# Kernel optimization log

Measured on AMD Instinct MI355X. Metric: run time of the kernel, lower is better.

Reference implementation:

```python
import jax, jax.numpy as jnp
import numpy as np

N_NODES = 32768
N_EDGES = 524288
N_FEAT = 256
HID = 256
N_GRAPHS = 64
N_CLASSES = 4
NODES_PER_GRAPH = N_NODES // N_GRAPHS
BN_EPS = 1e-5


def setup_inputs() -> dict:
    key = jax.random.key(0)
    ks = jax.random.split(key, 16)
    x = jax.random.normal(ks[0], (N_NODES, N_FEAT), dtype=jnp.float32)
    edge_index = jax.random.randint(ks[1], (2, N_EDGES), 0, N_NODES, dtype=jnp.int32)
    batch = (jnp.arange(N_NODES, dtype=jnp.int32) // NODES_PER_GRAPH)
    def xavier(k, shape):
        fan_in, fan_out = shape[0], shape[1]
        a = float(np.sqrt(6.0 / (fan_in + fan_out)))
        return jax.random.uniform(k, shape, jnp.float32, -a, a)
    return {
        "x": x, "edge_index": edge_index, "batch": batch,
        "W1": xavier(ks[2], (N_FEAT, HID)), "b1": jnp.zeros((HID,), jnp.float32),
        "g1": jnp.ones((HID,), jnp.float32), "be1": jnp.zeros((HID,), jnp.float32),
        "W2": xavier(ks[3], (HID, HID)), "b2": jnp.zeros((HID,), jnp.float32),
        "g2": jnp.ones((HID,), jnp.float32), "be2": jnp.zeros((HID,), jnp.float32),
        "W_ih": xavier(ks[4], (HID, 4 * HID)), "W_hh": xavier(ks[5], (HID, 4 * HID)),
        "b_ih": jnp.zeros((4 * HID,), jnp.float32), "b_hh": jnp.zeros((4 * HID,), jnp.float32),
        "W_fc": xavier(ks[6], (HID, N_CLASSES)), "b_fc": jnp.zeros((N_CLASSES,), jnp.float32),
    }


def gcn_conv(x, W, b, src, dst):
    # PyG GCNConv: add self-loops, symmetric normalization, aggregate, then bias
    h = x @ W                                   # [N, H]
    deg = jnp.zeros((x.shape[0],), h.dtype).at[dst].add(1.0) + 1.0  # in-deg + self-loop
    dinv = jax.lax.rsqrt(deg)
    coef = dinv[src] * dinv[dst]                # [E]
    msg = h[src] * coef[:, None]                # gather + scale, [E, H]
    agg = jnp.zeros_like(h).at[dst].add(msg)    # scatter-add
    agg = agg + h * (1.0 / deg)[:, None]        # self-loop term (norm = 1/deg)
    return agg + b


def batch_norm(x, gamma, beta):
    mean = jnp.mean(x, axis=0)
    var = jnp.mean(jnp.square(x - mean), axis=0)  # biased, as torch BN training
    return (x - mean) * jax.lax.rsqrt(var + BN_EPS) * gamma + beta


def reference(x, edge_index, batch, W1, b1, g1, be1, W2, b2, g2, be2,
              W_ih, W_hh, b_ih, b_hh, W_fc, b_fc):
    src, dst = edge_index[0], edge_index[1]
    h = jax.nn.relu(batch_norm(gcn_conv(x, W1, b1, src, dst), g1, be1))
    h = jax.nn.relu(batch_norm(gcn_conv(h, W2, b2, src, dst), g2, be2))
    # global mean pool over graphs
    sums = jax.ops.segment_sum(h, batch, num_segments=N_GRAPHS)
    cnts = jax.ops.segment_sum(jnp.ones((h.shape[0],), h.dtype), batch, num_segments=N_GRAPHS)
    pooled = sums / cnts[:, None]               # [G, H]
    # LSTM, seq_len = 1, zero initial state -> single cell step
    h0 = jnp.zeros((N_GRAPHS, HID), h.dtype)
    c0 = jnp.zeros((N_GRAPHS, HID), h.dtype)
    gates = pooled @ W_ih + h0 @ W_hh + b_ih + b_hh  # [G, 4H]
    i, f, g, o = jnp.split(gates, 4, axis=1)
    c1 = jax.nn.sigmoid(f) * c0 + jax.nn.sigmoid(i) * jnp.tanh(g)
    h1 = jax.nn.sigmoid(o) * jnp.tanh(c1)
    logits = h1 @ W_fc + b_fc
    logp = jax.nn.log_softmax(logits, axis=1)
    return (logp, (h1[None], c1[None]))
```

## Files before the change

### kernel.cpp

```cpp
#include <hip/hip_runtime.h>
#include <math.h>

#define N_NODES 32768
#define N_FEAT 256
#define HID 256
#define N_GRAPHS 64
#define NPG 512
#define N_CLASSES 4
#define BN_EPS 1e-5f

typedef __attribute__((ext_vector_type(8))) short bf16x8;
typedef __attribute__((ext_vector_type(4))) float f32x4;

__device__ __forceinline__ ushort f2b(float f) {
    union { float f; uint u; } v; v.f = f;
    uint u = v.u;
    return (ushort)((u + 0x7FFFu + ((u >> 16) & 1u)) >> 16);
}
__device__ __forceinline__ float bflo(uint u) {
    union { uint u; float f; } v; v.u = u << 16;
    return v.f;
}
__device__ __forceinline__ float bfhi(uint u) {
    union { uint u; float f; } v; v.u = u & 0xFFFF0000u;
    return v.f;
}

__global__ void k_count(const int* __restrict__ dst, int* __restrict__ degcnt, int E) {
    int e = blockIdx.x * 256 + threadIdx.x;
    if (e < E) atomicAdd(&degcnt[dst[e]], 1);
}

__global__ __launch_bounds__(1024) void k_scan_all(const int* __restrict__ degcnt,
                                                   float* __restrict__ dinv,
                                                   int* __restrict__ row_start,
                                                   int* __restrict__ cursor) {
    __shared__ int wsum[16];
    int t = threadIdx.x;
    int base = t * 32;
    int s = 0;
#pragma unroll
    for (int i = 0; i < 32; ++i) s += degcnt[base + i];
    int lane = t & 63, w = t >> 6;
    int v = s;
    for (int off = 1; off < 64; off <<= 1) {
        int u = __shfl_up(v, off);
        if (lane >= off) v += u;
    }
    if (lane == 63) wsum[w] = v;
    __syncthreads();
    if (t < 16) {
        int x = wsum[t];
        for (int off = 1; off < 16; off <<= 1) {
            int u = __shfl_up(x, off, 16);
            if (t >= off) x += u;
        }
        wsum[t] = x;
    }
    __syncthreads();
    int run = ((w > 0) ? wsum[w - 1] : 0) + v - s;
    for (int i = 0; i < 32; ++i) {
        int n = base + i;
        int c = degcnt[n];
        row_start[n] = run;
        cursor[n] = run;
        dinv[n] = rsqrtf((float)(c + 1));
        run += c;
    }
}

__global__ void k_fill(const int* __restrict__ src, const int* __restrict__ dst,
                       int* __restrict__ cursor, uint* __restrict__ csrs, int E) {
    int e = blockIdx.x * 256 + threadIdx.x;
    if (e >= E) return;
    int d = dst[e];
    int pos = atomicAdd(&cursor[d], 1);
    csrs[pos] = (uint)src[e];
}

__global__ void k_prep(const float* __restrict__ x, ushort* __restrict__ xb, int n8blk,
                       const float* __restrict__ W1, const float* __restrict__ W2,
                       ushort* __restrict__ Wt1, ushort* __restrict__ Wt2) {
    int b = blockIdx.x;
    if (b < n8blk) {
        int i = b * 256 + threadIdx.x;
        float4 v0 = *(const float4*)(x + (size_t)i * 8);
        float4 v1 = *(const float4*)(x + (size_t)i * 8 + 4);
        uint4 o;
        o.x = (uint)f2b(v0.x) | ((uint)f2b(v0.y) << 16);
        o.y = (uint)f2b(v0.z) | ((uint)f2b(v0.w) << 16);
        o.z = (uint)f2b(v1.x) | ((uint)f2b(v1.y) << 16);
        o.w = (uint)f2b(v1.z) | ((uint)f2b(v1.w) << 16);
        *(uint4*)(xb + (size_t)i * 8) = o;
    } else {
        int wb = b - n8blk;
        const float* W = (wb < 256) ? W1 : W2;
        ushort* Wt = (wb < 256) ? Wt1 : Wt2;
        int n = wb & 255;
        int k = threadIdx.x;
        Wt[n * 256 + k] = f2b(W[k * 256 + n]);
    }
}

__global__ __launch_bounds__(256) void k_gemm_bf16(const ushort* __restrict__ A,
                                                   const ushort* __restrict__ Bt,
                                                   const float* __restrict__ dinv,
                                                   ushort* __restrict__ hs) {
    int wid = threadIdx.x >> 6;
    int lane = threadIdx.x & 63;
    int m0 = blockIdx.y * 256 + wid * 64;
    int n0 = blockIdx.x * 64;
    int r = lane & 15;
    int ko = (lane >> 4) * 8;

    const ushort* Ab = A + (size_t)(m0 + r) * 256 + ko;
    const ushort* Bb = Bt + (size_t)(n0 + r) * 256 + ko;

    f32x4 acc[4][4] = {};
#pragma unroll
    for (int ks = 0; ks < 8; ++ks) {
        bf16x8 a[4], b[4];
#pragma unroll
        for (int i = 0; i < 4; ++i) {
            a[i] = *(const bf16x8*)(Ab + i * (16 * 256) + ks * 32);
            b[i] = *(const bf16x8*)(Bb + i * (16 * 256) + ks * 32);
        }
#pragma unroll
        for (int i = 0; i < 4; ++i)
#pragma unroll
            for (int j = 0; j < 4; ++j)
                acc[i][j] = __builtin_amdgcn_mfma_f32_16x16x32_bf16(a[i], b[j], acc[i][j], 0, 0, 0);
    }

    int rr = (lane >> 4) * 4;
    int cc = lane & 15;
#pragma unroll
    for (int i = 0; i < 4; ++i) {
        int row = m0 + i * 16 + rr;
#pragma unroll
        for (int r2 = 0; r2 < 4; ++r2) {
            float dv = dinv[row + r2];
#pragma unroll
            for (int j = 0; j < 4; ++j) {
                int col = n0 + j * 16 + cc;
                int slice = col >> 5;
                int within = col & 31;
                hs[(size_t)slice * (N_NODES * 32) + (size_t)(row + r2) * 32 + within] =
                    f2b(acc[i][j][r2] * dv);
            }
        }
    }
}

__global__ __launch_bounds__(256) void k_agg_bn(const ushort* __restrict__ hs,
                                                const uint* __restrict__ csrs,
                                                const int* __restrict__ row_start,
                                                const int* __restrict__ degcnt,
                                                const float* __restrict__ dinv,
                                                const float* __restrict__ bias,
                                                float* __restrict__ agg,
                                                float* __restrict__ bnsum,
                                                float* __restrict__ bnsq) {
    int slice = blockIdx.x & 7;
    int grp = blockIdx.x >> 3;
    int wid = threadIdx.x >> 6;
    int lane = threadIdx.x & 63;
    int j8 = lane >> 3;
    int fp = lane & 7;
    const ushort* hS = hs + (size_t)slice * (N_NODES * 32);

    float b0 = 0.f, b1 = 0.f, b2 = 0.f, b3 = 0.f;
    if (j8 == 0) {
        b0 = bias[slice * 32 + fp * 4 + 0];
        b1 = bias[slice * 32 + fp * 4 + 1];
        b2 = bias[slice * 32 + fp * 4 + 2];
        b3 = bias[slice * 32 + fp * 4 + 3];
    }

    float st[8] = {0.f, 0.f, 0.f, 0.f, 0.f, 0.f, 0.f, 0.f};

    for (int t = 0; t < 8; ++t) {
        int n = grp * 32 + wid * 8 + t;
        float dv = dinv[n];
        int base = row_start[n];
        int cnt = degcnt[n];
        float a0 = 0.f, a1 = 0.f, a2 = 0.f, a3 = 0.f;
        if (j8 == 0) {
            uint2 hv = *(const uint2*)(hS + (size_t)n * 32 + fp * 4);
            a0 = bflo(hv.x); a1 = bfhi(hv.x);
            a2 = bflo(hv.y); a3 = bfhi(hv.y);
        }
        int j = j8;
        for (; j + 8 < cnt; j += 16) {
            uint s0 = csrs[base + j];
            uint s1 = csrs[base + j + 8];
            uint2 h0 = *(const uint2*)(hS + (size_t)s0 * 32 + fp * 4);
            uint2 h1 = *(const uint2*)(hS + (size_t)s1 * 32 + fp * 4);
            a0 += bflo(h0.x) + bflo(h1.x);
            a1 += bfhi(h0.x) + bfhi(h1.x);
            a2 += bflo(h0.y) + bflo(h1.y);
            a3 += bfhi(h0.y) + bfhi(h1.y);
        }
        if (j < cnt) {
            uint s0 = csrs[base + j];
            uint2 h0 = *(const uint2*)(hS + (size_t)s0 * 32 + fp * 4);
            a0 += bflo(h0.x); a1 += bfhi(h0.x);
            a2 += bflo(h0.y); a3 += bfhi(h0.y);
        }
        a0 += __shfl_xor(a0, 8);  a1 += __shfl_xor(a1, 8);
        a2 += __shfl_xor(a2, 8);  a3 += __shfl_xor(a3, 8);
        a0 += __shfl_xor(a0, 16); a1 += __shfl_xor(a1, 16);
        a2 += __shfl_xor(a2, 16); a3 += __shfl_xor(a3, 16);
        a0 += __shfl_xor(a0, 32); a1 += __shfl_xor(a1, 32);
        a2 += __shfl_xor(a2, 32); a3 += __shfl_xor(a3, 32);
        if (j8 == 0) {
            float o0 = a0 * dv + b0;
            float o1 = a1 * dv + b1;
            float o2 = a2 * dv + b2;
            float o3 = a3 * dv + b3;
            *(float4*)&agg[(size_t)n * HID + slice * 32 + fp * 4] = make_float4(o0, o1, o2, o3);
            st[0] += o0; st[1] += o0 * o0;
            st[2] += o1; st[3] += o1 * o1;
            st[4] += o2; st[5] += o2 * o2;
            st[6] += o3; st[7] += o3 * o3;
        }
    }

    __shared__ float ls[4][8][8];
    if (j8 == 0) {
#pragma unroll
        for (int v = 0; v < 8; ++v) ls[wid][fp][v] = st[v];
    }
    __syncthreads();
    if (threadIdx.x < 64) {
        int f = threadIdx.x >> 3, v = threadIdx.x & 7;
        float tsum = ls[0][f][v] + ls[1][f][v] + ls[2][f][v] + ls[3][f][v];
        int feat = slice * 32 + f * 4 + (v >> 1);
        if ((v & 1) == 0) atomicAdd(&bnsum[feat], tsum);
        else              atomicAdd(&bnsq[feat], tsum);
    }
}

__global__ void k_bn_apply_b(const float* __restrict__ x, const float* __restrict__ bnsum,
                             const float* __restrict__ bnsq, const float* __restrict__ gamma,
                             const float* __restrict__ beta, ushort* __restrict__ out) {
    int i = blockIdx.x * 256 + threadIdx.x;
    if (i >= N_NODES * HID / 4) return;
    int f = (i & 63) * 4;
    const float invN = 1.0f / (float)N_NODES;
    float4 v = *(const float4*)(x + (size_t)i * 4);
    float r[4];
    float vv[4] = {v.x, v.y, v.z, v.w};
#pragma unroll
    for (int q = 0; q < 4; ++q) {
        float mean = bnsum[f + q] * invN;
        float var = bnsq[f + q] * invN - mean * mean;
        float t = (vv[q] - mean) * rsqrtf(var + BN_EPS) * gamma[f + q] + beta[f + q];
        r[q] = t > 0.0f ? t : 0.0f;
    }
    uint2 o;
    o.x = (uint)f2b(r[0]) | ((uint)f2b(r[1]) << 16);
    o.y = (uint)f2b(r[2]) | ((uint)f2b(r[3]) << 16);
    *(uint2*)(out + (size_t)i * 4) = o;
}

__global__ __launch_bounds__(256) void k_bn_pool(const float* __restrict__ agg,
                                                 const float* __restrict__ bnsum,
                                                 const float* __restrict__ bnsq,
                                                 const float* __restrict__ gamma,
                                                 const float* __restrict__ beta,
                                                 float* __restrict__ pooled) {
    int g = blockIdx.x >> 4;
    int blk = blockIdx.x & 15;
    int f = threadIdx.x;
    const float invN = 1.0f / (float)N_NODES;
    float mean = bnsum[f] * invN;
    float var = bnsq[f] * invN - mean * mean;
    float sc = rsqrtf(var + BN_EPS) * gamma[f];
    float sh = beta[f] - mean * sc;
    int r0 = g * NPG + blk * 32;
    float s = 0.0f;
#pragma unroll 4
    for (int r = 0; r < 32; ++r) {
        float v = agg[(size_t)(r0 + r) * HID + f] * sc + sh;
        s += v > 0.0f ? v : 0.0f;
    }
    atomicAdd(&pooled[g * HID + f], s);
}

__global__ __launch_bounds__(256) void k_head(const float* __restrict__ pooled,
                                              const float* __restrict__ W_ih,
                                              const float* __restrict__ b_ih,
                                              const float* __restrict__ b_hh,
                                              const float* __restrict__ W_fc,
                                              const float* __restrict__ b_fc,
                                              float* __restrict__ out) {
    __shared__ float p[HID];
    __shared__ float lsum[N_CLASSES][256];
    __shared__ float logits[N_CLASSES];
    int g = blockIdx.x, j = threadIdx.x;
    p[j] = pooled[g * HID + j] * (1.0f / (float)NPG);
    __syncthreads();

    float gi = 0.f, gf = 0.f, gg = 0.f, go = 0.f;
#pragma unroll 4
    for (int k = 0; k < HID; ++k) {
        float pk = p[k];
        const float* w = &W_ih[(size_t)k * (4 * HID) + j];
        gi += pk * w[0];
        gf += pk * w[HID];
        gg += pk * w[2 * HID];
        go += pk * w[3 * HID];
    }
    gi += b_ih[j] + b_hh[j];
    gf += b_ih[HID + j] + b_hh[HID + j];
    gg += b_ih[2 * HID + j] + b_hh[2 * HID + j];
    go += b_ih[3 * HID + j] + b_hh[3 * HID + j];
    (void)gf;

    float si = 1.f / (1.f + expf(-gi));
    float so = 1.f / (1.f + expf(-go));
    float c1 = si * tanhf(gg);
    float h1 = so * tanhf(c1);

    out[N_GRAPHS * N_CLASSES + g * HID + j] = h1;
    out[N_GRAPHS * N_CLASSES + N_GRAPHS * HID + g * HID + j] = c1;

#pragma unroll
    for (int c = 0; c < N_CLASSES; ++c)
        lsum[c][j] = h1 * W_fc[j * N_CLASSES + c];
    __syncthreads();
    for (int s = 128; s > 0; s >>= 1) {
        if (j < s) {
#pragma unroll
            for (int c = 0; c < N_CLASSES; ++c)
                lsum[c][j] += lsum[c][j + s];
        }
        __syncthreads();
    }
    if (j < N_CLASSES) logits[j] = lsum[j][0] + b_fc[j];
    __syncthreads();
    if (j < N_CLASSES) {
        float m = fmaxf(fmaxf(logits[0], logits[1]), fmaxf(logits[2], logits[3]));
        float lse = m + logf(expf(logits[0] - m) + expf(logits[1] - m) +
                             expf(logits[2] - m) + expf(logits[3] - m));
        out[g * N_CLASSES + j] = logits[j] - lse;
    }
}

extern "C" void kernel_launch(void* const* d_in, const int* in_sizes, int n_in,
                              void* d_out, int out_size, void* d_ws, size_t ws_size,
                              hipStream_t stream) {
    const float* x    = (const float*)d_in[0];
    const int*   ei   = (const int*)d_in[1];
    const float* W1   = (const float*)d_in[3];
    const float* b1   = (const float*)d_in[4];
    const float* g1   = (const float*)d_in[5];
    const float* be1  = (const float*)d_in[6];
    const float* W2   = (const float*)d_in[7];
    const float* b2   = (const float*)d_in[8];
    const float* g2   = (const float*)d_in[9];
    const float* be2  = (const float*)d_in[10];
    const float* W_ih = (const float*)d_in[11];
    const float* b_ih = (const float*)d_in[13];
    const float* b_hh = (const float*)d_in[14];
    const float* W_fc = (const float*)d_in[15];
    const float* b_fc = (const float*)d_in[16];
    float* out = (float*)d_out;

    int E = in_sizes[1] / 2;
    const int* src = ei;
    const int* dst = ei + E;

    const size_t MAT = (size_t)N_NODES * HID;
    float*  agg  = (float*)d_ws;
    ushort* xb   = (ushort*)(agg + MAT);
    ushort* hs   = xb + MAT;
    ushort* Wt1  = hs + MAT;
    ushort* Wt2  = Wt1 + 65536;
    float*  dinv = (float*)(Wt2 + 65536);
    int*    row_start = (int*)(dinv + N_NODES);
    int*    cursor    = row_start + N_NODES;
    uint*   csrs      = (uint*)(cursor + N_NODES);
    int*    degcnt = (int*)(csrs + E);
    float*  bn1sum = (float*)(degcnt + N_NODES);
    float*  bn1sq  = bn1sum + HID;
    float*  bn2sum = bn1sq + HID;
    float*  bn2sq  = bn2sum + HID;
    float*  pooled = bn2sq + HID;
    size_t zeroBytes = (size_t)N_NODES * 4 + 4 * HID * 4 + (size_t)N_GRAPHS * HID * 4;

    dim3 blk(256);
    int edgeBlocks = (E + 255) / 256;
    int n8blk = (int)(MAT / 8 / 256);
    int vec4Blocks = (int)(MAT / 4 / 256);
    dim3 gemmGrid(HID / 64, N_NODES / 256);

    hipMemsetAsync(degcnt, 0, zeroBytes, stream);

    k_count<<<edgeBlocks, blk, 0, stream>>>(dst, degcnt, E);
    k_scan_all<<<1, dim3(1024), 0, stream>>>(degcnt, dinv, row_start, cursor);
    k_fill<<<edgeBlocks, blk, 0, stream>>>(src, dst, cursor, csrs, E);
    k_prep<<<n8blk + 512, blk, 0, stream>>>(x, xb, n8blk, W1, W2, Wt1, Wt2);

    k_gemm_bf16<<<gemmGrid, blk, 0, stream>>>(xb, Wt1, dinv, hs);
    k_agg_bn<<<8192, blk, 0, stream>>>(hs, csrs, row_start, degcnt, dinv, b1, agg, bn1sum, bn1sq);
    k_bn_apply_b<<<vec4Blocks, blk, 0, stream>>>(agg, bn1sum, bn1sq, g1, be1, xb);

    k_gemm_bf16<<<gemmGrid, blk, 0, stream>>>(xb, Wt2, dinv, hs);
    k_agg_bn<<<8192, blk, 0, stream>>>(hs, csrs, row_start, degcnt, dinv, b2, agg, bn2sum, bn2sq);
    k_bn_pool<<<N_GRAPHS * 16, blk, 0, stream>>>(agg, bn2sum, bn2sq, g2, be2, pooled);

    k_head<<<N_GRAPHS, blk, 0, stream>>>(pooled, W_ih, b_ih, b_hh, W_fc, b_fc, out);
}
```

Baseline: 309.5 us.

## Use row-major bf16 features with whole-wave rows in aggregation and bf16 agg buffer

Stores the GEMM output row-major (256 features per node) instead of in 32-feature slices, so each wave processes a full node row, with 64 lanes covering 256 features and the edge loop unrolled by 8. This removes the 8x repeated traversal of the CSR indices across slices and the cross-lane shuffle reductions. The pre-BN aggregate is now stored as bf16 instead of fp32, halving its write and read traffic, at some precision cost before batch norm. Row degrees now come from row_start[n+1], so the separate degcnt load is dropped.

New measurement: 449.3 us. 1.45x slower.

```diff
diff --git a/kernel.cpp b/kernel.cpp
--- a/kernel.cpp
+++ b/kernel.cpp
@@ -67,6 +67,7 @@
         dinv[n] = rsqrtf((float)(c + 1));
         run += c;
     }
+    if (t == 0) row_start[N_NODES] = wsum[15];
 }
 
 __global__ void k_fill(const int* __restrict__ src, const int* __restrict__ dst,
@@ -143,10 +144,7 @@
 #pragma unroll
             for (int j = 0; j < 4; ++j) {
                 int col = n0 + j * 16 + cc;
-                int slice = col >> 5;
-                int within = col & 31;
-                hs[(size_t)slice * (N_NODES * 32) + (size_t)(row + r2) * 32 + within] =
-                    f2b(acc[i][j][r2] * dv);
+                hs[(size_t)(row + r2) * 256 + col] = f2b(acc[i][j][r2] * dv);
             }
         }
     }
@@ -155,108 +153,127 @@
 __global__ __launch_bounds__(256) void k_agg_bn(const ushort* __restrict__ hs,
                                                 const uint* __restrict__ csrs,
                                                 const int* __restrict__ row_start,
-                                                const int* __restrict__ degcnt,
                                                 const float* __restrict__ dinv,
                                                 const float* __restrict__ bias,
-                                                float* __restrict__ agg,
+                                                ushort* __restrict__ aggb,
                                                 float* __restrict__ bnsum,
                                                 float* __restrict__ bnsq) {
-    int slice = blockIdx.x & 7;
-    int grp = blockIdx.x >> 3;
     int wid = threadIdx.x >> 6;
     int lane = threadIdx.x & 63;
-    int j8 = lane >> 3;
-    int fp = lane & 7;
-    const ushort* hS = hs + (size_t)slice * (N_NODES * 32);
-
-    float b0 = 0.f, b1 = 0.f, b2 = 0.f, b3 = 0.f;
-    if (j8 == 0) {
-        b0 = bias[slice * 32 + fp * 4 + 0];
-        b1 = bias[slice * 32 + fp * 4 + 1];
-        b2 = bias[slice * 32 + fp * 4 + 2];
-        b3 = bias[slice * 32 + fp * 4 + 3];
-    }
-
-    float st[8] = {0.f, 0.f, 0.f, 0.f, 0.f, 0.f, 0.f, 0.f};
+    int foff = lane * 4;
+
+    float4 bv = *(const float4*)&bias[foff];
+    float bb[4] = {bv.x, bv.y, bv.z, bv.w};
+
+    float s[4] = {0.f, 0.f, 0.f, 0.f};
+    float q[4] = {0.f, 0.f, 0.f, 0.f};
 
     for (int t = 0; t < 8; ++t) {
-        int n = grp * 32 + wid * 8 + t;
+        int n = blockIdx.x * 32 + wid * 8 + t;
         float dv = dinv[n];
         int base = row_start[n];
-        int cnt = degcnt[n];
-        float a0 = 0.f, a1 = 0.f, a2 = 0.f, a3 = 0.f;
-        if (j8 == 0) {
-            uint2 hv = *(const uint2*)(hS + (size_t)n * 32 + fp * 4);
-            a0 = bflo(hv.x); a1 = bfhi(hv.x);
-            a2 = bflo(hv.y); a3 = bfhi(hv.y);
-        }
-        int j = j8;
-        for (; j + 8 < cnt; j += 16) {
+        int cnt = row_start[n + 1] - base;
+
+        uint2 hv = *(const uint2*)(hs + (size_t)n * 256 + foff);
+        float a0 = bflo(hv.x), a1 = bfhi(hv.x), a2 = bflo(hv.y), a3 = bfhi(hv.y);
+
+        int j = 0;
+        for (; j + 8 <= cnt; j += 8) {
+            uint s0 = csrs[base + j + 0];
+            uint s1 = csrs[base + j + 1];
+            uint s2 = csrs[base + j + 2];
+            uint s3 = csrs[base + j + 3];
+            uint s4 = csrs[base + j + 4];
+            uint s5 = csrs[base + j + 5];
+            uint s6 = csrs[base + j + 6];
+            uint s7 = csrs[base + j + 7];
+            uint2 h0 = *(const uint2*)(hs + (size_t)s0 * 256 + foff);
+            uint2 h1 = *(const uint2*)(hs + (size_t)s1 * 256 + foff);
+            uint2 h2 = *(const uint2*)(hs + (size_t)s2 * 256 + foff);
+            uint2 h3 = *(const uint2*)(hs + (size_t)s3 * 256 + foff);
+            uint2 h4 = *(const uint2*)(hs + (size_t)s4 * 256 + foff);
+            uint2 h5 = *(const uint2*)(hs + (size_t)s5 * 256 + foff);
+            uint2 h6 = *(const uint2*)(hs + (size_t)s6 * 256 + foff);
+            uint2 h7 = *(const uint2*)(hs + (size_t)s7 * 256 + foff);
+            a0 += bflo(h0.x) + bflo(h1.x) + bflo(h2.x) + bflo(h3.x)
+                + bflo(h4.x) + bflo(h5.x) + bflo(h6.x) + bflo(h7.x);
+            a1 += bfhi(h0.x) + bfhi(h1.x) + bfhi(h2.x) + bfhi(h3.x)
+                + bfhi(h4.x) + bfhi(h5.x) + bfhi(h6.x) + bfhi(h7.x);
+            a2 += bflo(h0.y) + bflo(h1.y) + bflo(h2.y) + bflo(h3.y)
+                + bflo(h4.y) + bflo(h5.y) + bflo(h6.y) + bflo(h7.y);
+            a3 += bfhi(h0.y) + bfhi(h1.y) + bfhi(h2.y) + bfhi(h3.y)
+                + bfhi(h4.y) + bfhi(h5.y) + bfhi(h6.y) + bfhi(h7.y);
+        }
+        for (; j + 4 <= cnt; j += 4) {
+            uint s0 = csrs[base + j + 0];
+            uint s1 = csrs[base + j + 1];
+            uint s2 = csrs[base + j + 2];
+            uint s3 = csrs[base + j + 3];
+            uint2 h0 = *(const uint2*)(hs + (size_t)s0 * 256 + foff);
+            uint2 h1 = *(const uint2*)(hs + (size_t)s1 * 256 + foff);
+            uint2 h2 = *(const uint2*)(hs + (size_t)s2 * 256 + foff);
+            uint2 h3 = *(const uint2*)(hs + (size_t)s3 * 256 + foff);
+            a0 += bflo(h0.x) + bflo(h1.x) + bflo(h2.x) + bflo(h3.x);
+            a1 += bfhi(h0.x) + bfhi(h1.x) + bfhi(h2.x) + bfhi(h3.x);
+            a2 += bflo(h0.y) + bflo(h1.y) + bflo(h2.y) + bflo(h3.y);
+            a3 += bfhi(h0.y) + bfhi(h1.y) + bfhi(h2.y) + bfhi(h3.y);
+        }
+        for (; j < cnt; ++j) {
             uint s0 = csrs[base + j];
-            uint s1 = csrs[base + j + 8];
-            uint2 h0 = *(const uint2*)(hS + (size_t)s0 * 32 + fp * 4);
-            uint2 h1 = *(const uint2*)(hS + (size_t)s1 * 32 + fp * 4);
-            a0 += bflo(h0.x) + bflo(h1.x);
-            a1 += bfhi(h0.x) + bfhi(h1.x);
-            a2 += bflo(h0.y) + bflo(h1.y);
-            a3 += bfhi(h0.y) + bfhi(h1.y);
-        }
-        if (j < cnt) {
-            uint s0 = csrs[base + j];
-            uint2 h0 = *(const uint2*)(hS + (size_t)s0 * 32 + fp * 4);
+            uint2 h0 = *(const uint2*)(hs + (size_t)s0 * 256 + foff);
             a0 += bflo(h0.x); a1 += bfhi(h0.x);
             a2 += bflo(h0.y); a3 += bfhi(h0.y);
         }
-        a0 += __shfl_xor(a0, 8);  a1 += __shfl_xor(a1, 8);
-        a2 += __shfl_xor(a2, 8);  a3 += __shfl_xor(a3, 8);
-        a0 += __shfl_xor(a0, 16); a1 += __shfl_xor(a1, 16);
-        a2 += __shfl_xor(a2, 16); a3 += __shfl_xor(a3, 16);
-        a0 += __shfl_xor(a0, 32); a1 += __shfl_xor(a1, 32);
-        a2 += __shfl_xor(a2, 32); a3 += __shfl_xor(a3, 32);
-        if (j8 == 0) {
-            float o0 = a0 * dv + b0;
-            float o1 = a1 * dv + b1;
-            float o2 = a2 * dv + b2;
-            float o3 = a3 * dv + b3;
-            *(float4*)&agg[(size_t)n * HID + slice * 32 + fp * 4] = make_float4(o0, o1, o2, o3);
-            st[0] += o0; st[1] += o0 * o0;
-            st[2] += o1; st[3] += o1 * o1;
-            st[4] += o2; st[5] += o2 * o2;
-            st[6] += o3; st[7] += o3 * o3;
-        }
-    }
-
-    __shared__ float ls[4][8][8];
-    if (j8 == 0) {
-#pragma unroll
-        for (int v = 0; v < 8; ++v) ls[wid][fp][v] = st[v];
-    }
+
+        float o0 = a0 * dv + bb[0];
+        float o1 = a1 * dv + bb[1];
+        float o2 = a2 * dv + bb[2];
+        float o3 = a3 * dv + bb[3];
+        ushort4 ov;
+        ov.x = f2b(o0); ov.y = f2b(o1); ov.z = f2b(o2); ov.w = f2b(o3);
+        *(ushort4*)(aggb + (size_t)n * HID + foff) = ov;
+        s[0] += o0; q[0] += o0 * o0;
+        s[1] += o1; q[1] += o1 * o1;
+        s[2] += o2; q[2] += o2 * o2;
+        s[3] += o3; q[3] += o3 * o3;
+    }
+
+    __shared__ float4 ssum[4][64];
+    __shared__ float4 ssq[4][64];
+    ssum[wid][lane] = make_float4(s[0], s[1], s[2], s[3]);
+    ssq[wid][lane] = make_float4(q[0], q[1], q[2], q[3]);
     __syncthreads();
     if (threadIdx.x < 64) {
-        int f = threadIdx.x >> 3, v = threadIdx.x & 7;
-        float tsum = ls[0][f][v] + ls[1][f][v] + ls[2][f][v] + ls[3][f][v];
-        int feat = slice * 32 + f * 4 + (v >> 1);
-        if ((v & 1) == 0) atomicAdd(&bnsum[feat], tsum);
-        else              atomicAdd(&bnsq[feat], tsum);
-    }
-}
-
-__global__ void k_bn_apply_b(const float* __restrict__ x, const float* __restrict__ bnsum,
+        float4 A = ssum[0][lane], B = ssq[0][lane];
+#pragma unroll
+        for (int w = 1; w < 4; ++w) {
+            float4 a2v = ssum[w][lane], b2v = ssq[w][lane];
+            A.x += a2v.x; A.y += a2v.y; A.z += a2v.z; A.w += a2v.w;
+            B.x += b2v.x; B.y += b2v.y; B.z += b2v.z; B.w += b2v.w;
+        }
+        atomicAdd(&bnsum[foff + 0], A.x); atomicAdd(&bnsq[foff + 0], B.x);
+        atomicAdd(&bnsum[foff + 1], A.y); atomicAdd(&bnsq[foff + 1], B.y);
+        atomicAdd(&bnsum[foff + 2], A.z); atomicAdd(&bnsq[foff + 2], B.z);
+        atomicAdd(&bnsum[foff + 3], A.w); atomicAdd(&bnsq[foff + 3], B.w);
+    }
+}
+
+__global__ void k_bn_apply_b(const ushort* __restrict__ x, const float* __restrict__ bnsum,
                              const float* __restrict__ bnsq, const float* __restrict__ gamma,
                              const float* __restrict__ beta, ushort* __restrict__ out) {
     int i = blockIdx.x * 256 + threadIdx.x;
     if (i >= N_NODES * HID / 4) return;
     int f = (i & 63) * 4;
     const float invN = 1.0f / (float)N_NODES;
-    float4 v = *(const float4*)(x + (size_t)i * 4);
+    uint2 v = *(const uint2*)(x + (size_t)i * 4);
+    float vv[4] = {bflo(v.x), bfhi(v.x), bflo(v.y), bfhi(v.y)};
     float r[4];
-    float vv[4] = {v.x, v.y, v.z, v.w};
-#pragma unroll
-    for (int q = 0; q < 4; ++q) {
-        float mean = bnsum[f + q] * invN;
-        float var = bnsq[f + q] * invN - mean * mean;
-        float t = (vv[q] - mean) * rsqrtf(var + BN_EPS) * gamma[f + q] + beta[f + q];
-        r[q] = t > 0.0f ? t : 0.0f;
+#pragma unroll
+    for (int qq = 0; qq < 4; ++qq) {
+        float mean = bnsum[f + qq] * invN;
+        float var = bnsq[f + qq] * invN - mean * mean;
+        float t = (vv[qq] - mean) * rsqrtf(var + BN_EPS) * gamma[f + qq] + beta[f + qq];
+        r[qq] = t > 0.0f ? t : 0.0f;
     }
     uint2 o;
     o.x = (uint)f2b(r[0]) | ((uint)f2b(r[1]) << 16);
@@ -264,7 +281,7 @@
     *(uint2*)(out + (size_t)i * 4) = o;
 }
 
-__global__ __launch_bounds__(256) void k_bn_pool(const float* __restrict__ agg,
+__global__ __launch_bounds__(256) void k_bn_pool(const ushort* __restrict__ aggb,
                                                  const float* __restrict__ bnsum,
                                                  const float* __restrict__ bnsq,
                                                  const float* __restrict__ gamma,
@@ -282,7 +299,7 @@
     float s = 0.0f;
 #pragma unroll 4
     for (int r = 0; r < 32; ++r) {
-        float v = agg[(size_t)(r0 + r) * HID + f] * sc + sh;
+        float v = bflo((uint)aggb[(size_t)(r0 + r) * HID + f]) * sc + sh;
         s += v > 0.0f ? v : 0.0f;
     }
     atomicAdd(&pooled[g * HID + f], s);
@@ -373,14 +390,14 @@
     const int* dst = ei + E;
 
     const size_t MAT = (size_t)N_NODES * HID;
-    float*  agg  = (float*)d_ws;
-    ushort* xb   = (ushort*)(agg + MAT);
+    ushort* aggb = (ushort*)d_ws;
+    ushort* xb   = aggb + MAT;
     ushort* hs   = xb + MAT;
     ushort* Wt1  = hs + MAT;
     ushort* Wt2  = Wt1 + 65536;
     float*  dinv = (float*)(Wt2 + 65536);
     int*    row_start = (int*)(dinv + N_NODES);
-    int*    cursor    = row_start + N_NODES;
+    int*    cursor    = row_start + N_NODES + 1;
     uint*   csrs      = (uint*)(cursor + N_NODES);
     int*    degcnt = (int*)(csrs + E);
     float*  bn1sum = (float*)(degcnt + N_NODES);
@@ -394,6 +411,7 @@
     int edgeBlocks = (E + 255) / 256;
     int n8blk = (int)(MAT / 8 / 256);
     int vec4Blocks = (int)(MAT / 4 / 256);
+    int aggBlocks = N_NODES / 32;
     dim3 gemmGrid(HID / 64, N_NODES / 256);
 
     hipMemsetAsync(degcnt, 0, zeroBytes, stream);
@@ -404,12 +422,12 @@
     k_prep<<<n8blk + 512, blk, 0, stream>>>(x, xb, n8blk, W1, W2, Wt1, Wt2);
 
     k_gemm_bf16<<<gemmGrid, blk, 0, stream>>>(xb, Wt1, dinv, hs);
-    k_agg_bn<<<8192, blk, 0, stream>>>(hs, csrs, row_start, degcnt, dinv, b1, agg, bn1sum, bn1sq);
-    k_bn_apply_b<<<vec4Blocks, blk, 0, stream>>>(agg, bn1sum, bn1sq, g1, be1, xb);
+    k_agg_bn<<<aggBlocks, blk, 0, stream>>>(hs, csrs, row_start, dinv, b1, aggb, bn1sum, bn1sq);
+    k_bn_apply_b<<<vec4Blocks, blk, 0, stream>>>(aggb, bn1sum, bn1sq, g1, be1, xb);
 
     k_gemm_bf16<<<gemmGrid, blk, 0, stream>>>(xb, Wt2, dinv, hs);
-    k_agg_bn<<<8192, blk, 0, stream>>>(hs, csrs, row_start, degcnt, dinv, b2, agg, bn2sum, bn2sq);
-    k_bn_pool<<<N_GRAPHS * 16, blk, 0, stream>>>(agg, bn2sum, bn2sq, g2, be2, pooled);
+    k_agg_bn<<<aggBlocks, blk, 0, stream>>>(hs, csrs, row_start, dinv, b2, aggb, bn2sum, bn2sq);
+    k_bn_pool<<<N_GRAPHS * 16, blk, 0, stream>>>(aggb, bn2sum, bn2sq, g2, be2, pooled);
 
     k_head<<<N_GRAPHS, blk, 0, stream>>>(pooled, W_ih, b_ih, b_hh, W_fc, b_fc, out);
 }
```
